# Performance work log

Hardware: AMD Instinct MI355X
Metric: run time of the kernel (lower is better)

The kernel has to match this reference:

```python
import jax, jax.numpy as jnp
import numpy as np

P, V, GRID = 64, 6890, 32
V_SUB = 256          # vertex subsample for the SDF-grid proxy
SCALE_FACTOR = 0.2   # forward() default
SDF_BAND = 0.15      # proxy: phi = relu(band - dist_to_surface) >= 0
N_FACES = 13776


def _trilinear(vol, pts):
    """torch grid_sample 3D, mode=bilinear, padding=zeros, align_corners=False.
    vol: [D,H,W]; pts: [...,3] with (x,y,z) in [-1,1] mapping to (W,H,D)."""
    D, H, W = vol.shape
    x = ((pts[..., 0] + 1.0) * W - 1.0) * 0.5
    y = ((pts[..., 1] + 1.0) * H - 1.0) * 0.5
    z = ((pts[..., 2] + 1.0) * D - 1.0) * 0.5
    x0 = jnp.floor(x).astype(jnp.int32); fx = x - x0
    y0 = jnp.floor(y).astype(jnp.int32); fy = y - y0
    z0 = jnp.floor(z).astype(jnp.int32); fz = z - z0

    def corner(xi, yi, zi, w):
        inb = (xi >= 0) & (xi < W) & (yi >= 0) & (yi < H) & (zi >= 0) & (zi < D)
        v = vol[jnp.clip(zi, 0, D - 1), jnp.clip(yi, 0, H - 1), jnp.clip(xi, 0, W - 1)]
        return jnp.where(inb, v, 0.0) * w

    return (corner(x0,     y0,     z0,     (1 - fx) * (1 - fy) * (1 - fz))
          + corner(x0 + 1, y0,     z0,     fx       * (1 - fy) * (1 - fz))
          + corner(x0,     y0 + 1, z0,     (1 - fx) * fy       * (1 - fz))
          + corner(x0 + 1, y0 + 1, z0,     fx       * fy       * (1 - fz))
          + corner(x0,     y0,     z0 + 1, (1 - fx) * (1 - fy) * fz)
          + corner(x0 + 1, y0,     z0 + 1, fx       * (1 - fy) * fz)
          + corner(x0,     y0 + 1, z0 + 1, (1 - fx) * fy       * fz)
          + corner(x0 + 1, y0 + 1, z0 + 1, fx       * fy       * fz))


def _compute_phi(verts_cs):
    """Deterministic non-negative SDF-grid proxy (stands in for the external
    SDF CUDA op; original computes it under no_grad). verts_cs: [P,V,3] in [-1,1].
    Returns phi: [P,GRID,GRID,GRID] (D,H,W indexing)."""
    # cell centers in normalized coords (align_corners=False convention)
    lin = (2.0 * jnp.arange(GRID, dtype=verts_cs.dtype) + 1.0) / GRID - 1.0
    zz, yy, xx = jnp.meshgrid(lin, lin, lin, indexing='ij')
    gp = jnp.stack([xx, yy, zz], axis=-1).reshape(-1, 3)  # [G^3,3] (x,y,z)
    stride = V // V_SUB
    sub = verts_cs[:, ::stride, :][:, :V_SUB]             # [P,V_SUB,3]

    def per_person(v):  # v: [V_SUB,3]
        d2 = jnp.sum((gp[:, None, :] - v[None, :, :]) ** 2, axis=-1)  # [G^3,V_SUB]
        d = jnp.sqrt(jnp.min(d2, axis=-1))
        return jnp.maximum(SDF_BAND - d, 0.0).reshape(GRID, GRID, GRID)

    return jax.lax.map(per_person, sub)  # sequential over people: bounds peak memory


def _forward(vertices, translation):
    sg = jax.lax.stop_gradient
    verts = vertices + translation[:, None, :]                      # [P,V,3]
    n = verts.shape[0]
    bmin = sg(jnp.min(verts, axis=1))                               # [P,3] (no_grad bboxes)
    bmax = sg(jnp.max(verts, axis=1))
    # overlap(i,j) per axis: not (min_i > max_j or min_j > max_i)
    ov = jnp.all((bmin[:, None, :] <= bmax[None, :, :]) &
                 (bmin[None, :, :] <= bmax[:, None, :]), axis=-1)   # [P,P], diag True
    # faithful to original ~filter_isolated_boxes: kept only if overlapping ALL others
    valid = jnp.all(ov, axis=1)                                     # [P]
    nv = jnp.sum(valid.astype(verts.dtype))
    center = (bmin + bmax) * 0.5                                    # [P,3]
    scale = (1.0 + SCALE_FACTOR) * 0.5 * jnp.max(bmax - bmin, axis=-1)  # [P]
    verts_cs = sg((verts - center[:, None, :]) / scale[:, None, None])
    phi = sg(_compute_phi(verts_cs))                                # [P,G,G,G]
    # coordinates of ALL people's vertices in person-i's grid frame: [P,P,V,3]
    loc = (verts[None, :, :, :] - center[:, None, None, :]) / scale[:, None, None, None]
    phi_val = jax.vmap(_trilinear)(phi, loc.reshape(n, n * V, 3)).reshape(n, n, V)
    # pair (i,j) contributes iff both valid and i != j (weights[i]=0 in the loop)
    pair_w = (valid[:, None] & valid[None, :] & ~jnp.eye(n, dtype=bool)).astype(verts.dtype)
    denom = jnp.maximum(nv, 1.0) ** 2
    return jnp.sum(pair_w * jnp.sum(phi_val, axis=-1)) / denom


def setup_inputs() -> dict:
    key = jax.random.key(0)
    k1, k2, k3 = jax.random.split(key, 3)
    vertices = jax.random.normal(k1, (P, V, 3), dtype=jnp.float32) * 0.2
    translation = jax.random.uniform(k2, (P, 3), dtype=jnp.float32, minval=-0.3, maxval=0.3)
    faces = jax.random.randint(k3, (N_FACES, 3), 0, V, dtype=jnp.int32)
    return {"vertices": vertices, "translation": translation, "faces": faces}


def reference(vertices, translation, faces):
    # faces only feed the external SDF op (replaced by the phi proxy); unused here
    return _forward(vertices, translation)
```

## Files before the change

kernel.cpp:

```cpp
#include <hip/hip_runtime.h>


#define NP 64
#define NVERT 6890
#define NV3 (NVERT*3)
#define GRD 32
#define QDIM 34
#define QPLANE (QDIM*QDIM)
#define QVOL (QDIM*QPLANE)
#define VSUB 256
#define VSTRIDE 26
#define BAND 0.15f
#define PHI_SCALE 64.0f
#define INV_PHI_SCALE 0.015625f
#define LDS_BYTES (QVOL*2 + 64)
#define SAMPLE_BLOCKS (8*NP)

typedef float floatx2 __attribute__((ext_vector_type(2)));

__device__ __forceinline__ float wave_min(float v) {
  #pragma unroll
  for (int off = 32; off > 0; off >>= 1) v = fminf(v, __shfl_down(v, off));
  return v;
}
__device__ __forceinline__ float wave_max(float v) {
  #pragma unroll
  for (int off = 32; off > 0; off >>= 1) v = fmaxf(v, __shfl_down(v, off));
  return v;
}
__device__ __forceinline__ float wave_sum(float v) {
  #pragma unroll
  for (int off = 32; off > 0; off >>= 1) v += __shfl_down(v, off);
  return v;
}

__global__ __launch_bounds__(1024) void k_phi(
    const float* __restrict__ verts, const float* __restrict__ trans,
    unsigned short* __restrict__ pairs, float* __restrict__ bbox,
    float* __restrict__ accp, unsigned int* __restrict__ donep) {
  int p = blockIdx.x >> 2;
  int zq = blockIdx.x & 3;
  int tid = threadIdx.x;
  int x = tid & 31, y = tid >> 5;

  __shared__ float kv[VSUB][3];
  __shared__ float phib[8][32][32];
  __shared__ float s[16][6];
  __shared__ float bbf[6];
  __shared__ int nkeep;

  if (blockIdx.x == 0 && tid == 0) { accp[0] = 0.0f; donep[0] = 0u; }

  const float* vp = verts + (size_t)p * NV3;
  float tx = trans[p*3+0], ty = trans[p*3+1], tz = trans[p*3+2];
  float mnx=1e30f, mny=1e30f, mnz=1e30f, mxx=-1e30f, mxy=-1e30f, mxz=-1e30f;
  for (int v = tid; v < NVERT; v += 1024) {
    float xx = vp[v*3+0]+tx, yy = vp[v*3+1]+ty, zz = vp[v*3+2]+tz;
    mnx=fminf(mnx,xx); mny=fminf(mny,yy); mnz=fminf(mnz,zz);
    mxx=fmaxf(mxx,xx); mxy=fmaxf(mxy,yy); mxz=fmaxf(mxz,zz);
  }
  mnx=wave_min(mnx); mny=wave_min(mny); mnz=wave_min(mnz);
  mxx=wave_max(mxx); mxy=wave_max(mxy); mxz=wave_max(mxz);
  int wave = tid >> 6, lane = tid & 63;
  if (lane == 0) {
    s[wave][0]=mnx; s[wave][1]=mny; s[wave][2]=mnz;
    s[wave][3]=mxx; s[wave][4]=mxy; s[wave][5]=mxz;
  }
  __syncthreads();
  if (tid == 0) {
    float a0=s[0][0],a1=s[0][1],a2=s[0][2],b0=s[0][3],b1=s[0][4],b2=s[0][5];
    for (int w = 1; w < 16; ++w) {
      a0=fminf(a0,s[w][0]); a1=fminf(a1,s[w][1]); a2=fminf(a2,s[w][2]);
      b0=fmaxf(b0,s[w][3]); b1=fmaxf(b1,s[w][4]); b2=fmaxf(b2,s[w][5]);
    }
    bbf[0]=a0; bbf[1]=a1; bbf[2]=a2; bbf[3]=b0; bbf[4]=b1; bbf[5]=b2;
    bbox[p*3+0]=a0; bbox[p*3+1]=a1; bbox[p*3+2]=a2;
    bbox[192+p*3+0]=b0; bbox[192+p*3+1]=b1; bbox[192+p*3+2]=b2;
    nkeep = 0;
  }
  __syncthreads();

  float cx = 0.5f*(bbf[0]+bbf[3]), cy = 0.5f*(bbf[1]+bbf[4]);
  float cz = 0.5f*(bbf[2]+bbf[5]);
  float ext = fmaxf(bbf[3]-bbf[0], fmaxf(bbf[4]-bbf[1], bbf[5]-bbf[2]));
  float is = 1.0f / (0.6f * ext);
  const float inv = 1.0f / (float)GRD;

  if (tid < VSUB) {
    int v = tid * VSTRIDE;
    const float* vv = vp + (size_t)v * 3;
    float X = (vv[0] + tx - cx) * is;
    float Y = (vv[1] + ty - cy) * is;
    float Z = (vv[2] + tz - cz) * is;
    float zlo = (2.0f*(zq*8)     + 1.0f) * inv - 1.0f;
    float zhi = (2.0f*(zq*8 + 7) + 1.0f) * inv - 1.0f;
    float dz = fmaxf(fmaxf(zlo - Z, Z - zhi), 0.0f);
    if (dz < BAND) {
      int idx = atomicAdd(&nkeep, 1);
      kv[idx][0] = X; kv[idx][1] = Y; kv[idx][2] = Z;
    }
  }
  __syncthreads();
  int nk = nkeep;

  float gx = (2.0f*x + 1.0f) * inv - 1.0f;
  float gy = (2.0f*y + 1.0f) * inv - 1.0f;
  float gz[8];
  #pragma unroll
  for (int k = 0; k < 8; ++k) gz[k] = (2.0f*(zq*8+k) + 1.0f) * inv - 1.0f;

  float d2[8];
  #pragma unroll
  for (int k = 0; k < 8; ++k) d2[k] = 1e30f;

  int w = tid >> 6;
  float ylo = (4.0f*w + 1.0f) * inv - 1.0f;
  float yhi = (4.0f*w + 3.0f) * inv - 1.0f;

  for (int v = 0; v < nk; ++v) {
    float Y = kv[v][1];
    if (fmaxf(ylo - Y, Y - yhi) >= BAND) continue;
    float dx = gx - kv[v][0];
    float dy = gy - Y;
    float vz = kv[v][2];
    float r2 = fmaf(dy, dy, dx*dx);
    #pragma unroll
    for (int k = 0; k < 8; ++k) {
      float dz = gz[k] - vz;
      d2[k] = fminf(d2[k], fmaf(dz, dz, r2));
    }
  }
  #pragma unroll
  for (int k = 0; k < 8; ++k)
    phib[k][y][x] = fmaxf(BAND - sqrtf(d2[k]), 0.0f) * PHI_SCALE;
  __syncthreads();

  unsigned short* qp = pairs + (size_t)p * QVOL;
  for (int idx = tid; idx < QPLANE; idx += 1024) {
    int iy = idx / QDIM, ix = idx % QDIM;
    int gyy = iy - 1, gxx = ix - 1;
    bool gyok = (unsigned)gyy < 32u;
    bool aok = gyok && ((unsigned)gxx < 32u);
    bool bok = gyok && ((unsigned)ix  < 32u);
    int ya = gyok ? gyy : 0;
    int xa = aok ? gxx : 0;
    int xb = bok ? ix : 0;
    #pragma unroll
    for (int k = 0; k < 8; ++k) {
      float a = aok ? phib[k][ya][xa] : 0.0f;
      float b = bok ? phib[k][ya][xb] : 0.0f;
      int pk = __builtin_amdgcn_cvt_pk_fp8_f32(a, b, 0, false);
      qp[(zq*8 + k + 1)*QPLANE + idx] = (unsigned short)(pk & 0xffff);
    }
    if (zq == 0) qp[idx] = 0;
    if (zq == 3) qp[33*QPLANE + idx] = 0;
  }
}

__device__ __forceinline__ float qsample(const unsigned short* q,
                                         float X, float Y, float Z) {
  X = fminf(fmaxf(X, 0.0f), 33.99f);
  Y = fminf(fmaxf(Y, 0.0f), 32.999f);
  Z = fminf(fmaxf(Z, 0.0f), 32.999f);
  float xf = floorf(X), yf = floorf(Y), zf = floorf(Z);
  float fx = X - xf, fy = Y - yf, fz = Z - zf;
  int e = ((int)zf * QDIM + (int)yf) * QDIM + (int)xf;
  unsigned int w00 = q[e];
  unsigned int w10 = q[e + QDIM];
  unsigned int w01 = q[e + QPLANE];
  unsigned int w11 = q[e + QPLANE + QDIM];
  floatx2 c00 = __builtin_amdgcn_cvt_pk_f32_fp8((int)w00, false);
  floatx2 c10 = __builtin_amdgcn_cvt_pk_f32_fp8((int)w10, false);
  floatx2 c01 = __builtin_amdgcn_cvt_pk_f32_fp8((int)w01, false);
  floatx2 c11 = __builtin_amdgcn_cvt_pk_f32_fp8((int)w11, false);
  float u00 = fmaf(fx, c00.y - c00.x, c00.x);
  float u10 = fmaf(fx, c10.y - c10.x, c10.x);
  float u01 = fmaf(fx, c01.y - c01.x, c01.x);
  float u11 = fmaf(fx, c11.y - c11.x, c11.x);
  float a0 = fmaf(fy, u10 - u00, u00);
  float a1 = fmaf(fy, u11 - u01, u01);
  return fmaf(fz, a1 - a0, a0);
}

__global__ __launch_bounds__(896, 7) void k_sample(
    const float* __restrict__ verts, const float* __restrict__ trans,
    const float* __restrict__ bbox, const unsigned short* __restrict__ pairs,
    float* __restrict__ accp, unsigned int* __restrict__ donep,
    float* __restrict__ out) {
  extern __shared__ unsigned char smem[];
  const unsigned short* sq = (const unsigned short*)smem;
  float* red = (float*)(smem + (size_t)QVOL * 2);

  int i = blockIdx.y;
  int tid = threadIdx.x;
  int lane = tid & 63;

  float amn0 = bbox[lane*3+0], amn1 = bbox[lane*3+1], amn2 = bbox[lane*3+2];
  float amx0 = bbox[192+lane*3+0], amx1 = bbox[192+lane*3+1],
        amx2 = bbox[192+lane*3+2];
  bool valid = true;
  for (int j = 0; j < NP; ++j) {
    valid = valid && (amn0 <= bbox[192+j*3+0]) && (bbox[j*3+0] <= amx0)
                  && (amn1 <= bbox[192+j*3+1]) && (bbox[j*3+1] <= amx1)
                  && (amn2 <= bbox[192+j*3+2]) && (bbox[j*3+2] <= amx2);
  }
  unsigned long long mask = __ballot(valid);
  int nvi = (int)__popcll(mask);
  bool active = (mask >> i) & 1ull;

  float bx0 = bbox[i*3+0], by0 = bbox[i*3+1], bz0 = bbox[i*3+2];
  float bx1 = bbox[192+i*3+0], by1 = bbox[192+i*3+1], bz1 = bbox[192+i*3+2];
  float ext = fmaxf(bx1-bx0, fmaxf(by1-by0, bz1-bz0));
  float s16 = 16.0f / (0.6f * ext);
  float cx = 0.5f*(bx0+bx1), cy = 0.5f*(by0+by1), cz = 0.5f*(bz0+bz1);

  if (active && nvi > 1) {
    {
      const uint4* src = (const uint4*)(pairs + (size_t)i * QVOL);
      uint4* dst = (uint4*)smem;
      for (int t = tid; t < QVOL/8; t += 896) dst[t] = src[t];
    }
    __syncthreads();

    int v = blockIdx.x * 896 + tid;
    bool ok = v < NVERT;
    int vc = ok ? v : 0;
    float bx = fmaf(-cx, s16, 16.5f) + (ok ? 0.0f : 1e9f);
    float by = fmaf(-cy, s16, 16.5f);
    float bz = fmaf(-cz, s16, 16.5f);

    float acc = 0.0f;
    #pragma unroll 2
    for (int jj = 0; jj < NP; ++jj) {
      if (jj == i || !((mask >> jj) & 1ull)) continue;
      const float* vj = verts + ((size_t)jj * NVERT + vc) * 3;
      float vx = vj[0], vy = vj[1], vz = vj[2];
      float oxj = fmaf(trans[jj*3+0], s16, bx);
      float oyj = fmaf(trans[jj*3+1], s16, by);
      float ozj = fmaf(trans[jj*3+2], s16, bz);
      acc += qsample(sq, fmaf(vx, s16, oxj), fmaf(vy, s16, oyj),
                     fmaf(vz, s16, ozj));
    }

    acc = wave_sum(acc);
    int wv = tid >> 6;
    if (lane == 0) red[wv] = acc;
    __syncthreads();
    if (tid == 0) {
      float tot = 0.0f;
      #pragma unroll
      for (int w = 0; w < 14; ++w) tot += red[w];
      atomicAdd(accp, tot * INV_PHI_SCALE);
    }
  }

  if (tid == 0) {
    __threadfence();
    unsigned int old = atomicAdd(donep, 1u);
    if (old == SAMPLE_BLOCKS - 1) {
      float nv = fmaxf((float)nvi, 1.0f);
      float loss = atomicAdd(accp, 0.0f);
      out[0] = loss / (nv * nv);
    }
  }
}

extern "C" void kernel_launch(void* const* d_in, const int* in_sizes, int n_in,
                              void* d_out, int out_size, void* d_ws, size_t ws_size,
                              hipStream_t stream) {
  const float* verts = (const float*)d_in[0];
  const float* trans = (const float*)d_in[1];
  float* out = (float*)d_out;

  unsigned short* pairs = (unsigned short*)d_ws;
  float* bbox      = (float*)((unsigned char*)d_ws + (size_t)NP * QVOL * 2);
  float* accp      = bbox + 384;
  unsigned int* donep = (unsigned int*)(accp + 1);

  hipFuncSetAttribute((const void*)k_sample,
                      hipFuncAttributeMaxDynamicSharedMemorySize, LDS_BYTES);

  k_phi<<<NP*4, 1024, 0, stream>>>(verts, trans, pairs, bbox, accp, donep);
  k_sample<<<dim3(8, NP), 896, LDS_BYTES, stream>>>(verts, trans, bbox, pairs,
                                                    accp, donep, out);
}
```

Baseline: 118.3 us.

## Write translated vertices in SoA layout and prefetch LDS grid before validity check

New measurement: 126.6 us. 1.07x slower.

```diff
diff --git a/kernel.cpp b/kernel.cpp
--- a/kernel.cpp
+++ b/kernel.cpp
@@ -4,6 +4,7 @@
 #define NP 64
 #define NVERT 6890
 #define NV3 (NVERT*3)
+#define QCH 1723
 #define GRD 32
 #define QDIM 34
 #define QPLANE (QDIM*QDIM)
@@ -36,8 +37,9 @@
 
 __global__ __launch_bounds__(1024) void k_phi(
     const float* __restrict__ verts, const float* __restrict__ trans,
-    unsigned short* __restrict__ pairs, float* __restrict__ bbox,
-    float* __restrict__ accp, unsigned int* __restrict__ donep) {
+    unsigned short* __restrict__ pairs, float* __restrict__ vertsT,
+    float* __restrict__ bbox, float* __restrict__ accp,
+    unsigned int* __restrict__ donep) {
   int p = blockIdx.x >> 2;
   int zq = blockIdx.x & 3;
   int tid = threadIdx.x;
@@ -58,6 +60,16 @@
     float xx = vp[v*3+0]+tx, yy = vp[v*3+1]+ty, zz = vp[v*3+2]+tz;
     mnx=fminf(mnx,xx); mny=fminf(mny,yy); mnz=fminf(mnz,zz);
     mxx=fmaxf(mxx,xx); mxy=fmaxf(mxy,yy); mxz=fmaxf(mxz,zz);
+  }
+  {
+    float* o0 = vertsT + (size_t)(p*3+0) * NVERT;
+    float* o1 = vertsT + (size_t)(p*3+1) * NVERT;
+    float* o2 = vertsT + (size_t)(p*3+2) * NVERT;
+    int q0 = zq * QCH;
+    int q1 = q0 + QCH; if (q1 > NVERT) q1 = NVERT;
+    for (int v = q0 + tid; v < q1; v += 1024) {
+      o0[v] = vp[v*3+0]+tx; o1[v] = vp[v*3+1]+ty; o2[v] = vp[v*3+2]+tz;
+    }
   }
   mnx=wave_min(mnx); mny=wave_min(mny); mnz=wave_min(mnz);
   mxx=wave_max(mxx); mxy=wave_max(mxy); mxz=wave_max(mxz);
@@ -183,10 +195,9 @@
 }
 
 __global__ __launch_bounds__(896, 7) void k_sample(
-    const float* __restrict__ verts, const float* __restrict__ trans,
-    const float* __restrict__ bbox, const unsigned short* __restrict__ pairs,
-    float* __restrict__ accp, unsigned int* __restrict__ donep,
-    float* __restrict__ out) {
+    const float* __restrict__ vertsT, const float* __restrict__ bbox,
+    const unsigned short* __restrict__ pairs, float* __restrict__ accp,
+    unsigned int* __restrict__ donep, float* __restrict__ out) {
   extern __shared__ unsigned char smem[];
   const unsigned short* sq = (const unsigned short*)smem;
   float* red = (float*)(smem + (size_t)QVOL * 2);
@@ -194,6 +205,12 @@
   int i = blockIdx.y;
   int tid = threadIdx.x;
   int lane = tid & 63;
+
+  {
+    const uint4* src = (const uint4*)(pairs + (size_t)i * QVOL);
+    uint4* dst = (uint4*)smem;
+    for (int t = tid; t < QVOL/8; t += 896) dst[t] = src[t];
+  }
 
   float amn0 = bbox[lane*3+0], amn1 = bbox[lane*3+1], amn2 = bbox[lane*3+2];
   float amx0 = bbox[192+lane*3+0], amx1 = bbox[192+lane*3+1],
@@ -213,15 +230,9 @@
   float ext = fmaxf(bx1-bx0, fmaxf(by1-by0, bz1-bz0));
   float s16 = 16.0f / (0.6f * ext);
   float cx = 0.5f*(bx0+bx1), cy = 0.5f*(by0+by1), cz = 0.5f*(bz0+bz1);
+  __syncthreads();
 
   if (active && nvi > 1) {
-    {
-      const uint4* src = (const uint4*)(pairs + (size_t)i * QVOL);
-      uint4* dst = (uint4*)smem;
-      for (int t = tid; t < QVOL/8; t += 896) dst[t] = src[t];
-    }
-    __syncthreads();
-
     int v = blockIdx.x * 896 + tid;
     bool ok = v < NVERT;
     int vc = ok ? v : 0;
@@ -233,13 +244,11 @@
     #pragma unroll 2
     for (int jj = 0; jj < NP; ++jj) {
       if (jj == i || !((mask >> jj) & 1ull)) continue;
-      const float* vj = verts + ((size_t)jj * NVERT + vc) * 3;
-      float vx = vj[0], vy = vj[1], vz = vj[2];
-      float oxj = fmaf(trans[jj*3+0], s16, bx);
-      float oyj = fmaf(trans[jj*3+1], s16, by);
-      float ozj = fmaf(trans[jj*3+2], s16, bz);
-      acc += qsample(sq, fmaf(vx, s16, oxj), fmaf(vy, s16, oyj),
-                     fmaf(vz, s16, ozj));
+      const float* p0 = vertsT + (size_t)(jj*3) * NVERT;
+      float X = fmaf(p0[vc],         s16, bx);
+      float Y = fmaf(p0[NVERT+vc],   s16, by);
+      float Z = fmaf(p0[2*NVERT+vc], s16, bz);
+      acc += qsample(sq, X, Y, Z);
     }
 
     acc = wave_sum(acc);
@@ -273,14 +282,16 @@
   float* out = (float*)d_out;
 
   unsigned short* pairs = (unsigned short*)d_ws;
-  float* bbox      = (float*)((unsigned char*)d_ws + (size_t)NP * QVOL * 2);
+  float* vertsT    = (float*)((unsigned char*)d_ws + (size_t)NP * QVOL * 2);
+  float* bbox      = vertsT + (size_t)NP * NV3;
   float* accp      = bbox + 384;
   unsigned int* donep = (unsigned int*)(accp + 1);
 
   hipFuncSetAttribute((const void*)k_sample,
                       hipFuncAttributeMaxDynamicSharedMemorySize, LDS_BYTES);
 
-  k_phi<<<NP*4, 1024, 0, stream>>>(verts, trans, pairs, bbox, accp, donep);
-  k_sample<<<dim3(8, NP), 896, LDS_BYTES, stream>>>(verts, trans, bbox, pairs,
+  k_phi<<<NP*4, 1024, 0, stream>>>(verts, trans, pairs, vertsT, bbox,
+                                   accp, donep);
+  k_sample<<<dim3(8, NP), 896, LDS_BYTES, stream>>>(vertsT, bbox, pairs,
                                                     accp, donep, out);
 }
```
